# Kernel tuning notes

Measured on AMD Instinct MI355X. Metric: run time of the kernel, lower is better.

Reference implementation:

```python
import jax, jax.numpy as jnp
import numpy as np


def setup_inputs() -> dict:
    key = jax.random.key(0)
    k1, k2 = jax.random.split(key)
    B, H, N, C = 8, 8, 2048, 64
    x = jax.random.normal(k1, (B, H, N, C), dtype=jnp.float32)
    # torch nn.Linear(dim, 3*dim) weight layout: [3C, C]
    W_qkv = jax.random.normal(k2, (3 * C, C), dtype=jnp.float32) * (C ** -0.5)
    return {"x": x, "W_qkv": W_qkv}


def reference(x, W_qkv):
    B, H, N, C = x.shape
    scale = C ** -0.5
    # fused qkv projection: x @ W^T, then split
    qkv = jnp.einsum('bhnc,dc->bhnd', x, W_qkv)  # [B,H,N,3C]
    q, k, v = jnp.split(qkv, 3, axis=-1)
    # full N x N score matrix (matches the naive original)
    attn = jnp.einsum('bhnc,bhmc->bhnm', q, k) * scale
    attn = jax.nn.softmax(attn, axis=-1)
    out = jnp.einsum('bhnm,bhmc->bhnc', attn, v)  # [B,H,N,C]
    # head-mixing shuffle: reshape(B,H,N,H,C//H).transpose(1,3).reshape(B,H,N,C)
    out = out.reshape(B, H, N, H, C // H)
    out = out.transpose(0, 3, 2, 1, 4)
    return out.reshape(B, H, N, C)
```

## Files before the change

### kernel.cpp

```cpp
#include <hip/hip_runtime.h>
#include <math.h>

#define BH    64
#define NSEQ  2048
#define CDIM  64
#define KSTR  72
#define VLS   136

typedef unsigned short ushort_t;
typedef __attribute__((ext_vector_type(8))) short short8;
typedef __attribute__((ext_vector_type(4))) float float4v;

__device__ __forceinline__ ushort_t f32_to_bf16_rne(float x) {
  unsigned int u = __float_as_uint(x);
  u += 0x7fffu + ((u >> 16) & 1u);
  return (ushort_t)(u >> 16);
}

__device__ __forceinline__ void glds16(const ushort_t* g, ushort_t* l) {
  __builtin_amdgcn_global_load_lds(
      (const __attribute__((address_space(1))) void*)g,
      (__attribute__((address_space(3))) void*)l, 16, 0, 0);
}

__global__ __launch_bounds__(256) void qkv_proj_mfma(
    const float* __restrict__ x, const float* __restrict__ w,
    ushort_t* __restrict__ q, ushort_t* __restrict__ k,
    ushort_t* __restrict__ vt) {
  __shared__ ushort_t Wb[192 * KSTR];
  __shared__ ushort_t Vl[64 * VLS];
  const int t = threadIdx.x;
  const int lane = t & 63, wv = t >> 6;
  const int quad = lane >> 4, l16 = lane & 15;
  const long rowbase = (long)blockIdx.x * 128;
  const int head  = (int)(rowbase >> 11);
  const int nbase = (int)(rowbase & 2047);

  for (int u = t; u < 1536; u += 256) {
    const int d = u >> 3, o8 = (u & 7) * 8;
    const float sc = (d < 64) ? 0.1803368801111244f : 1.0f;
    const float4 f0 = *reinterpret_cast<const float4*>(w + d * 64 + o8);
    const float4 f1 = *reinterpret_cast<const float4*>(w + d * 64 + o8 + 4);
    ushort_t tmp[8] __attribute__((aligned(16)));
    tmp[0] = f32_to_bf16_rne(f0.x * sc); tmp[1] = f32_to_bf16_rne(f0.y * sc);
    tmp[2] = f32_to_bf16_rne(f0.z * sc); tmp[3] = f32_to_bf16_rne(f0.w * sc);
    tmp[4] = f32_to_bf16_rne(f1.x * sc); tmp[5] = f32_to_bf16_rne(f1.y * sc);
    tmp[6] = f32_to_bf16_rne(f1.z * sc); tmp[7] = f32_to_bf16_rne(f1.w * sc);
    *reinterpret_cast<uint4*>(&Wb[d * KSTR + o8]) = *reinterpret_cast<const uint4*>(tmp);
  }
  __syncthreads();

  short8 xf[2][2];
#pragma unroll
  for (int tm = 0; tm < 2; ++tm)
#pragma unroll
    for (int kb = 0; kb < 2; ++kb) {
      const float* xp = x + (rowbase + wv * 32 + tm * 16 + l16) * 64 + kb * 32 + quad * 8;
      const float4 f0 = *reinterpret_cast<const float4*>(xp);
      const float4 f1 = *reinterpret_cast<const float4*>(xp + 4);
      ushort_t tmp[8] __attribute__((aligned(16)));
      tmp[0] = f32_to_bf16_rne(f0.x); tmp[1] = f32_to_bf16_rne(f0.y);
      tmp[2] = f32_to_bf16_rne(f0.z); tmp[3] = f32_to_bf16_rne(f0.w);
      tmp[4] = f32_to_bf16_rne(f1.x); tmp[5] = f32_to_bf16_rne(f1.y);
      tmp[6] = f32_to_bf16_rne(f1.z); tmp[7] = f32_to_bf16_rne(f1.w);
      xf[tm][kb] = *reinterpret_cast<const short8*>(tmp);
    }

  float4v acc[2][12];
#pragma unroll
  for (int tm = 0; tm < 2; ++tm)
#pragma unroll
    for (int nt = 0; nt < 12; ++nt)
#pragma unroll
      for (int r = 0; r < 4; ++r) acc[tm][nt][r] = 0.f;

#pragma unroll
  for (int kb = 0; kb < 2; ++kb)
#pragma unroll
    for (int nt = 0; nt < 12; ++nt) {
      const short8 wf = *reinterpret_cast<const short8*>(
          &Wb[(nt * 16 + l16) * KSTR + kb * 32 + quad * 8]);
      acc[0][nt] = __builtin_amdgcn_mfma_f32_16x16x32_bf16(xf[0][kb], wf, acc[0][nt], 0, 0, 0);
      acc[1][nt] = __builtin_amdgcn_mfma_f32_16x16x32_bf16(xf[1][kb], wf, acc[1][nt], 0, 0, 0);
    }

#pragma unroll
  for (int tm = 0; tm < 2; ++tm)
#pragma unroll
    for (int nt = 0; nt < 12; ++nt)
#pragma unroll
      for (int r = 0; r < 4; ++r) {
        const int row_local = wv * 32 + tm * 16 + quad * 4 + r;
        const ushort_t val = f32_to_bf16_rne(acc[tm][nt][r]);
        const int d = nt * 16 + l16;
        if (nt < 4)      q[(rowbase + row_local) * 64 + d] = val;
        else if (nt < 8) k[(rowbase + row_local) * 64 + (d - 64)] = val;
        else             Vl[(d - 128) * VLS + row_local] = val;
      }
  __syncthreads();

#pragma unroll
  for (int i = 0; i < 4; ++i) {
    const int uidx = t + i * 256;
    const int c = uidx >> 4, n0 = (uidx & 15) * 8;
    *reinterpret_cast<uint4*>(vt + (long)head * (64 * 2048) + (long)c * 2048 + nbase + n0) =
        *reinterpret_cast<const uint4*>(&Vl[c * VLS + n0]);
  }
}

__global__ __launch_bounds__(256, 3) void flash_attn_mfma(
    const ushort_t* __restrict__ q, const ushort_t* __restrict__ k,
    const ushort_t* __restrict__ vt, float* __restrict__ out) {
  __shared__ ushort_t Ks2[2][64 * 64];
  __shared__ ushort_t Vs2[2][64 * 64];
  __shared__ ushort_t Ps[128 * KSTR];
  const int t = threadIdx.x;
  const int lane = t & 63, w = t >> 6;
  const int quad = lane >> 4, l16 = lane & 15;
  const int id = blockIdx.x;
  const int qt = id >> 6;
  const int bh = ((id & 7) << 3) | ((id >> 3) & 7);
  const long hoff = (long)bh * NSEQ * CDIM;
  const ushort_t* qp  = q  + hoff + (long)qt * 128 * CDIM;
  const ushort_t* kp  = k  + hoff;
  const ushort_t* vtp = vt + hoff;

  short8 qf[2][2];
#pragma unroll
  for (int tm = 0; tm < 2; ++tm)
#pragma unroll
    for (int kb = 0; kb < 2; ++kb)
      qf[tm][kb] = *reinterpret_cast<const short8*>(
          qp + (w * 32 + tm * 16 + l16) * 64 + kb * 32 + quad * 8);

  float4v O[4][2];
  float rs[2];
#pragma unroll
  for (int tm = 0; tm < 2; ++tm) rs[tm] = 0.f;
#pragma unroll
  for (int ct = 0; ct < 4; ++ct)
#pragma unroll
    for (int tm = 0; tm < 2; ++tm)
#pragma unroll
      for (int r = 0; r < 4; ++r) O[ct][tm][r] = 0.f;

  const int srow = w * 16 + (lane >> 3);
  const int schk = (lane & 7) ^ (lane >> 3);
  const int sdst = w * 16 * 64;

#pragma unroll
  for (int j = 0; j < 2; ++j) {
    glds16(kp + (long)(srow + j * 8) * 64 + schk * 8, &Ks2[0][sdst + j * 512]);
    glds16(vtp + (long)(srow + j * 8) * 2048 + schk * 8, &Vs2[0][sdst + j * 512]);
  }

  for (int tile = 0; tile < NSEQ / 64; ++tile) {
    const int cur = tile & 1;
    __syncthreads();
    if (tile < NSEQ / 64 - 1) {
      const long nxt = tile + 1;
#pragma unroll
      for (int j = 0; j < 2; ++j) {
        glds16(kp + (nxt * 64 + srow + j * 8) * 64 + schk * 8,
               &Ks2[1 - cur][sdst + j * 512]);
        glds16(vtp + (long)(srow + j * 8) * 2048 + nxt * 64 + schk * 8,
               &Vs2[1 - cur][sdst + j * 512]);
      }
    }

    float4v s[4][2];
#pragma unroll
    for (int nt = 0; nt < 4; ++nt)
#pragma unroll
      for (int tm = 0; tm < 2; ++tm)
#pragma unroll
        for (int r = 0; r < 4; ++r) s[nt][tm][r] = 0.f;

#pragma unroll
    for (int kb = 0; kb < 2; ++kb) {
      short8 kf[4];
#pragma unroll
      for (int nt = 0; nt < 4; ++nt)
        kf[nt] = *reinterpret_cast<const short8*>(
            &Ks2[cur][(nt * 16 + l16) * 64 + (((kb * 4 + quad) ^ (l16 & 7)) * 8)]);
#pragma unroll
      for (int nt = 0; nt < 4; ++nt)
#pragma unroll
        for (int tm = 0; tm < 2; ++tm)
          s[nt][tm] = __builtin_amdgcn_mfma_f32_16x16x32_bf16(
              kf[nt], qf[tm][kb], s[nt][tm], 0, 0, 0);
    }

#pragma unroll
    for (int tm = 0; tm < 2; ++tm)
#pragma unroll
      for (int nt = 0; nt < 4; ++nt) {
        float p0 = __builtin_amdgcn_exp2f(s[nt][tm][0]);
        float p1 = __builtin_amdgcn_exp2f(s[nt][tm][1]);
        float p2 = __builtin_amdgcn_exp2f(s[nt][tm][2]);
        float p3 = __builtin_amdgcn_exp2f(s[nt][tm][3]);
        rs[tm] += (p0 + p1) + (p2 + p3);
        uint2 pk;
        pk.x = ((__float_as_uint(p0) + 0x8000u) >> 16) |
               ((__float_as_uint(p1) + 0x8000u) & 0xffff0000u);
        pk.y = ((__float_as_uint(p2) + 0x8000u) >> 16) |
               ((__float_as_uint(p3) + 0x8000u) & 0xffff0000u);
        *reinterpret_cast<uint2*>(
            &Ps[(w * 32 + tm * 16 + l16) * KSTR + nt * 16 + quad * 4]) = pk;
      }

#pragma unroll
    for (int kb = 0; kb < 2; ++kb) {
      short8 pf[2], vf[4];
#pragma unroll
      for (int tm = 0; tm < 2; ++tm)
        pf[tm] = *reinterpret_cast<const short8*>(
            &Ps[(w * 32 + tm * 16 + l16) * KSTR + kb * 32 + quad * 8]);
#pragma unroll
      for (int ct = 0; ct < 4; ++ct)
        vf[ct] = *reinterpret_cast<const short8*>(
            &Vs2[cur][(ct * 16 + l16) * 64 + (((kb * 4 + quad) ^ (l16 & 7)) * 8)]);
#pragma unroll
      for (int ct = 0; ct < 4; ++ct)
#pragma unroll
        for (int tm = 0; tm < 2; ++tm)
          O[ct][tm] = __builtin_amdgcn_mfma_f32_16x16x32_bf16(
              vf[ct], pf[tm], O[ct][tm], 0, 0, 0);
    }
  }

  const int bi = bh >> 3, h = bh & 7;
  float inv[2];
#pragma unroll
  for (int tm = 0; tm < 2; ++tm) {
    float l = rs[tm];
    l += __shfl_xor(l, 16, 64);
    l += __shfl_xor(l, 32, 64);
    inv[tm] = 1.f / l;
  }
#pragma unroll
  for (int ct = 0; ct < 4; ++ct)
#pragma unroll
    for (int tm = 0; tm < 2; ++tm) {
      const int n = qt * 128 + w * 32 + tm * 16 + l16;
      const int h2 = ct * 2 + (quad >> 1);
      const int c2b = (quad & 1) * 4;
      float4 v4;
      v4.x = O[ct][tm][0] * inv[tm]; v4.y = O[ct][tm][1] * inv[tm];
      v4.z = O[ct][tm][2] * inv[tm]; v4.w = O[ct][tm][3] * inv[tm];
      *reinterpret_cast<float4*>(
          &out[(((long)(bi * 8 + h2)) * NSEQ + n) * 64 + h * 8 + c2b]) = v4;
    }
}

extern "C" void kernel_launch(void* const* d_in, const int* in_sizes, int n_in,
                              void* d_out, int out_size, void* d_ws, size_t ws_size,
                              hipStream_t stream) {
  (void)in_sizes; (void)n_in; (void)out_size; (void)ws_size;
  const float* x = (const float*)d_in[0];
  const float* w = (const float*)d_in[1];
  float* out = (float*)d_out;

  ushort_t* qws  = (ushort_t*)d_ws;
  ushort_t* kws  = qws + (size_t)BH * NSEQ * CDIM;
  ushort_t* vtws = kws + (size_t)BH * NSEQ * CDIM;

  qkv_proj_mfma<<<(BH * NSEQ) / 128, 256, 0, stream>>>(x, w, qws, kws, vtws);
  flash_attn_mfma<<<1024, 256, 0, stream>>>(qws, kws, vtws, out);
}
```

Before: 202.0 us.

## Double query tile per block, shrink KV tile, and transpose projection outputs in registers

The attention kernel now gives each wave 64 query rows (256 per block, 512 blocks) and streams K/V in 32-key tiles with a new swizzled P layout. Each loaded K/V tile is therefore reused across more queries, which cuts LDS and global traffic per FLOP, at the cost of more registers and lower occupancy (launch bound lowered to 2). The projection kernel swaps MFMA operand order so Q/K and transposed V are written as packed 4-element vectors straight from registers. This drops the LDS staging buffer and one barrier. The grid shrinks to 512 blocks, which may leave fewer waves to hide latency on the GPU's many CUs.

```diff
diff --git a/kernel.cpp b/kernel.cpp
--- a/kernel.cpp
+++ b/kernel.cpp
@@ -4,8 +4,7 @@
 #define BH    64
 #define NSEQ  2048
 #define CDIM  64
-#define KSTR  72
-#define VLS   136
+#define WSTR  72
 
 typedef unsigned short ushort_t;
 typedef __attribute__((ext_vector_type(8))) short short8;
@@ -17,6 +16,11 @@
   return (ushort_t)(u >> 16);
 }
 
+__device__ __forceinline__ unsigned int pk2(float a, float b) {
+  return ((__float_as_uint(a) + 0x8000u) >> 16) |
+         ((__float_as_uint(b) + 0x8000u) & 0xffff0000u);
+}
+
 __device__ __forceinline__ void glds16(const ushort_t* g, ushort_t* l) {
   __builtin_amdgcn_global_load_lds(
       (const __attribute__((address_space(1))) void*)g,
@@ -27,8 +31,7 @@
     const float* __restrict__ x, const float* __restrict__ w,
     ushort_t* __restrict__ q, ushort_t* __restrict__ k,
     ushort_t* __restrict__ vt) {
-  __shared__ ushort_t Wb[192 * KSTR];
-  __shared__ ushort_t Vl[64 * VLS];
+  __shared__ ushort_t Wb[192 * WSTR];
   const int t = threadIdx.x;
   const int lane = t & 63, wv = t >> 6;
   const int quad = lane >> 4, l16 = lane & 15;
@@ -46,7 +49,7 @@
     tmp[2] = f32_to_bf16_rne(f0.z * sc); tmp[3] = f32_to_bf16_rne(f0.w * sc);
     tmp[4] = f32_to_bf16_rne(f1.x * sc); tmp[5] = f32_to_bf16_rne(f1.y * sc);
     tmp[6] = f32_to_bf16_rne(f1.z * sc); tmp[7] = f32_to_bf16_rne(f1.w * sc);
-    *reinterpret_cast<uint4*>(&Wb[d * KSTR + o8]) = *reinterpret_cast<const uint4*>(tmp);
+    *reinterpret_cast<uint4*>(&Wb[d * WSTR + o8]) = *reinterpret_cast<const uint4*>(tmp);
   }
   __syncthreads();
 
@@ -66,54 +69,72 @@
       xf[tm][kb] = *reinterpret_cast<const short8*>(tmp);
     }
 
-  float4v acc[2][12];
+  float4v aqk[8][2];
+  float4v av[2][4];
+#pragma unroll
+  for (int nt = 0; nt < 8; ++nt)
+#pragma unroll
+    for (int tm = 0; tm < 2; ++tm)
+#pragma unroll
+      for (int r = 0; r < 4; ++r) aqk[nt][tm][r] = 0.f;
 #pragma unroll
   for (int tm = 0; tm < 2; ++tm)
 #pragma unroll
-    for (int nt = 0; nt < 12; ++nt)
-#pragma unroll
-      for (int r = 0; r < 4; ++r) acc[tm][nt][r] = 0.f;
-
-#pragma unroll
-  for (int kb = 0; kb < 2; ++kb)
-#pragma unroll
-    for (int nt = 0; nt < 12; ++nt) {
+    for (int nt = 0; nt < 4; ++nt)
+#pragma unroll
+      for (int r = 0; r < 4; ++r) av[tm][nt][r] = 0.f;
+
+#pragma unroll
+  for (int kb = 0; kb < 2; ++kb) {
+#pragma unroll
+    for (int nt = 0; nt < 8; ++nt) {
       const short8 wf = *reinterpret_cast<const short8*>(
-          &Wb[(nt * 16 + l16) * KSTR + kb * 32 + quad * 8]);
-      acc[0][nt] = __builtin_amdgcn_mfma_f32_16x16x32_bf16(xf[0][kb], wf, acc[0][nt], 0, 0, 0);
-      acc[1][nt] = __builtin_amdgcn_mfma_f32_16x16x32_bf16(xf[1][kb], wf, acc[1][nt], 0, 0, 0);
-    }
-
+          &Wb[(nt * 16 + l16) * WSTR + kb * 32 + quad * 8]);
+      aqk[nt][0] = __builtin_amdgcn_mfma_f32_16x16x32_bf16(wf, xf[0][kb], aqk[nt][0], 0, 0, 0);
+      aqk[nt][1] = __builtin_amdgcn_mfma_f32_16x16x32_bf16(wf, xf[1][kb], aqk[nt][1], 0, 0, 0);
+    }
+#pragma unroll
+    for (int nt = 0; nt < 4; ++nt) {
+      const short8 wfv = *reinterpret_cast<const short8*>(
+          &Wb[((128 + nt * 16) + l16) * WSTR + kb * 32 + quad * 8]);
+      av[0][nt] = __builtin_amdgcn_mfma_f32_16x16x32_bf16(xf[0][kb], wfv, av[0][nt], 0, 0, 0);
+      av[1][nt] = __builtin_amdgcn_mfma_f32_16x16x32_bf16(xf[1][kb], wfv, av[1][nt], 0, 0, 0);
+    }
+  }
+
+#pragma unroll
+  for (int tm = 0; tm < 2; ++tm) {
+    const long row = rowbase + wv * 32 + tm * 16 + l16;
+#pragma unroll
+    for (int nt = 0; nt < 8; ++nt) {
+      uint2 pk;
+      pk.x = pk2(aqk[nt][tm][0], aqk[nt][tm][1]);
+      pk.y = pk2(aqk[nt][tm][2], aqk[nt][tm][3]);
+      if (nt < 4)
+        *reinterpret_cast<uint2*>(q + row * 64 + nt * 16 + quad * 4) = pk;
+      else
+        *reinterpret_cast<uint2*>(k + row * 64 + (nt - 4) * 16 + quad * 4) = pk;
+    }
+  }
 #pragma unroll
   for (int tm = 0; tm < 2; ++tm)
 #pragma unroll
-    for (int nt = 0; nt < 12; ++nt)
-#pragma unroll
-      for (int r = 0; r < 4; ++r) {
-        const int row_local = wv * 32 + tm * 16 + quad * 4 + r;
-        const ushort_t val = f32_to_bf16_rne(acc[tm][nt][r]);
-        const int d = nt * 16 + l16;
-        if (nt < 4)      q[(rowbase + row_local) * 64 + d] = val;
-        else if (nt < 8) k[(rowbase + row_local) * 64 + (d - 64)] = val;
-        else             Vl[(d - 128) * VLS + row_local] = val;
-      }
-  __syncthreads();
-
-#pragma unroll
-  for (int i = 0; i < 4; ++i) {
-    const int uidx = t + i * 256;
-    const int c = uidx >> 4, n0 = (uidx & 15) * 8;
-    *reinterpret_cast<uint4*>(vt + (long)head * (64 * 2048) + (long)c * 2048 + nbase + n0) =
-        *reinterpret_cast<const uint4*>(&Vl[c * VLS + n0]);
-  }
-}
-
-__global__ __launch_bounds__(256, 3) void flash_attn_mfma(
+    for (int nt = 0; nt < 4; ++nt) {
+      const int c = nt * 16 + l16;
+      uint2 pk;
+      pk.x = pk2(av[tm][nt][0], av[tm][nt][1]);
+      pk.y = pk2(av[tm][nt][2], av[tm][nt][3]);
+      *reinterpret_cast<uint2*>(vt + (long)head * (64 * 2048) + (long)c * 2048 +
+                                nbase + wv * 32 + tm * 16 + quad * 4) = pk;
+    }
+}
+
+__global__ __launch_bounds__(256, 2) void flash_attn_mfma(
     const ushort_t* __restrict__ q, const ushort_t* __restrict__ k,
     const ushort_t* __restrict__ vt, float* __restrict__ out) {
-  __shared__ ushort_t Ks2[2][64 * 64];
-  __shared__ ushort_t Vs2[2][64 * 64];
-  __shared__ ushort_t Ps[128 * KSTR];
+  __shared__ ushort_t Ks2[2][32 * 64];
+  __shared__ ushort_t Vs2[2][64 * 32];
+  __shared__ ushort_t Ps[256 * 32];
   const int t = threadIdx.x;
   const int lane = t & 63, w = t >> 6;
   const int quad = lane >> 4, l16 = lane & 15;
@@ -121,118 +142,112 @@
   const int qt = id >> 6;
   const int bh = ((id & 7) << 3) | ((id >> 3) & 7);
   const long hoff = (long)bh * NSEQ * CDIM;
-  const ushort_t* qp  = q  + hoff + (long)qt * 128 * CDIM;
+  const ushort_t* qp  = q  + hoff + (long)qt * 256 * CDIM;
   const ushort_t* kp  = k  + hoff;
   const ushort_t* vtp = vt + hoff;
 
-  short8 qf[2][2];
-#pragma unroll
-  for (int tm = 0; tm < 2; ++tm)
+  short8 qf[4][2];
+#pragma unroll
+  for (int tm = 0; tm < 4; ++tm)
 #pragma unroll
     for (int kb = 0; kb < 2; ++kb)
       qf[tm][kb] = *reinterpret_cast<const short8*>(
-          qp + (w * 32 + tm * 16 + l16) * 64 + kb * 32 + quad * 8);
-
-  float4v O[4][2];
-  float rs[2];
-#pragma unroll
-  for (int tm = 0; tm < 2; ++tm) rs[tm] = 0.f;
+          qp + (w * 64 + tm * 16 + l16) * 64 + kb * 32 + quad * 8);
+
+  float4v O[4][4];
+  float rs[4];
+#pragma unroll
+  for (int tm = 0; tm < 4; ++tm) rs[tm] = 0.f;
 #pragma unroll
   for (int ct = 0; ct < 4; ++ct)
 #pragma unroll
-    for (int tm = 0; tm < 2; ++tm)
+    for (int tm = 0; tm < 4; ++tm)
 #pragma unroll
       for (int r = 0; r < 4; ++r) O[ct][tm][r] = 0.f;
 
-  const int srow = w * 16 + (lane >> 3);
-  const int schk = (lane & 7) ^ (lane >> 3);
-  const int sdst = w * 16 * 64;
-
-#pragma unroll
-  for (int j = 0; j < 2; ++j) {
-    glds16(kp + (long)(srow + j * 8) * 64 + schk * 8, &Ks2[0][sdst + j * 512]);
-    glds16(vtp + (long)(srow + j * 8) * 2048 + schk * 8, &Vs2[0][sdst + j * 512]);
-  }
-
-  for (int tile = 0; tile < NSEQ / 64; ++tile) {
+  const int krow = w * 8 + (lane >> 3);
+  const int kchk = (lane & 7) ^ (lane >> 3);
+  const int kdst = w * 8 * 64;
+  const int vrow = w * 16 + (lane >> 2);
+  const int vchk = (lane & 3) ^ ((lane >> 3) & 3);
+  const int vdst = w * 16 * 32;
+  const int pswz = (l16 >> 1) & 3;
+
+  glds16(kp + (long)krow * 64 + kchk * 8, &Ks2[0][kdst]);
+  glds16(vtp + (long)vrow * 2048 + vchk * 8, &Vs2[0][vdst]);
+
+  for (int tile = 0; tile < NSEQ / 32; ++tile) {
     const int cur = tile & 1;
     __syncthreads();
-    if (tile < NSEQ / 64 - 1) {
+    if (tile < NSEQ / 32 - 1) {
       const long nxt = tile + 1;
-#pragma unroll
-      for (int j = 0; j < 2; ++j) {
-        glds16(kp + (nxt * 64 + srow + j * 8) * 64 + schk * 8,
-               &Ks2[1 - cur][sdst + j * 512]);
-        glds16(vtp + (long)(srow + j * 8) * 2048 + nxt * 64 + schk * 8,
-               &Vs2[1 - cur][sdst + j * 512]);
-      }
-    }
-
-    float4v s[4][2];
-#pragma unroll
-    for (int nt = 0; nt < 4; ++nt)
-#pragma unroll
-      for (int tm = 0; tm < 2; ++tm)
+      glds16(kp + (nxt * 32 + krow) * 64 + kchk * 8, &Ks2[1 - cur][kdst]);
+      glds16(vtp + (long)vrow * 2048 + nxt * 32 + vchk * 8, &Vs2[1 - cur][vdst]);
+    }
+
+    float4v s[2][4];
+#pragma unroll
+    for (int nt = 0; nt < 2; ++nt)
+#pragma unroll
+      for (int tm = 0; tm < 4; ++tm)
 #pragma unroll
         for (int r = 0; r < 4; ++r) s[nt][tm][r] = 0.f;
 
 #pragma unroll
     for (int kb = 0; kb < 2; ++kb) {
-      short8 kf[4];
-#pragma unroll
-      for (int nt = 0; nt < 4; ++nt)
+      short8 kf[2];
+#pragma unroll
+      for (int nt = 0; nt < 2; ++nt)
         kf[nt] = *reinterpret_cast<const short8*>(
             &Ks2[cur][(nt * 16 + l16) * 64 + (((kb * 4 + quad) ^ (l16 & 7)) * 8)]);
 #pragma unroll
-      for (int nt = 0; nt < 4; ++nt)
-#pragma unroll
-        for (int tm = 0; tm < 2; ++tm)
+      for (int nt = 0; nt < 2; ++nt)
+#pragma unroll
+        for (int tm = 0; tm < 4; ++tm)
           s[nt][tm] = __builtin_amdgcn_mfma_f32_16x16x32_bf16(
               kf[nt], qf[tm][kb], s[nt][tm], 0, 0, 0);
     }
 
 #pragma unroll
-    for (int tm = 0; tm < 2; ++tm)
-#pragma unroll
-      for (int nt = 0; nt < 4; ++nt) {
-        float p0 = __builtin_amdgcn_exp2f(s[nt][tm][0]);
-        float p1 = __builtin_amdgcn_exp2f(s[nt][tm][1]);
-        float p2 = __builtin_amdgcn_exp2f(s[nt][tm][2]);
-        float p3 = __builtin_amdgcn_exp2f(s[nt][tm][3]);
+    for (int tm = 0; tm < 4; ++tm)
+#pragma unroll
+      for (int nt = 0; nt < 2; ++nt) {
+        const float p0 = __builtin_amdgcn_exp2f(s[nt][tm][0]);
+        const float p1 = __builtin_amdgcn_exp2f(s[nt][tm][1]);
+        const float p2 = __builtin_amdgcn_exp2f(s[nt][tm][2]);
+        const float p3 = __builtin_amdgcn_exp2f(s[nt][tm][3]);
         rs[tm] += (p0 + p1) + (p2 + p3);
         uint2 pk;
-        pk.x = ((__float_as_uint(p0) + 0x8000u) >> 16) |
-               ((__float_as_uint(p1) + 0x8000u) & 0xffff0000u);
-        pk.y = ((__float_as_uint(p2) + 0x8000u) >> 16) |
-               ((__float_as_uint(p3) + 0x8000u) & 0xffff0000u);
+        pk.x = pk2(p0, p1);
+        pk.y = pk2(p2, p3);
         *reinterpret_cast<uint2*>(
-            &Ps[(w * 32 + tm * 16 + l16) * KSTR + nt * 16 + quad * 4]) = pk;
+            &Ps[(w * 64 + tm * 16 + l16) * 32 +
+                (((nt * 2 + (quad >> 1)) ^ pswz) * 8) + (quad & 1) * 4]) = pk;
       }
 
-#pragma unroll
-    for (int kb = 0; kb < 2; ++kb) {
-      short8 pf[2], vf[4];
-#pragma unroll
-      for (int tm = 0; tm < 2; ++tm)
+    {
+      short8 pf[4], vf[4];
+#pragma unroll
+      for (int tm = 0; tm < 4; ++tm)
         pf[tm] = *reinterpret_cast<const short8*>(
-            &Ps[(w * 32 + tm * 16 + l16) * KSTR + kb * 32 + quad * 8]);
+            &Ps[(w * 64 + tm * 16 + l16) * 32 + ((quad ^ pswz) * 8)]);
 #pragma unroll
       for (int ct = 0; ct < 4; ++ct)
         vf[ct] = *reinterpret_cast<const short8*>(
-            &Vs2[cur][(ct * 16 + l16) * 64 + (((kb * 4 + quad) ^ (l16 & 7)) * 8)]);
+            &Vs2[cur][(ct * 16 + l16) * 32 + ((quad ^ pswz) * 8)]);
 #pragma unroll
       for (int ct = 0; ct < 4; ++ct)
 #pragma unroll
-        for (int tm = 0; tm < 2; ++tm)
+        for (int tm = 0; tm < 4; ++tm)
           O[ct][tm] = __builtin_amdgcn_mfma_f32_16x16x32_bf16(
               vf[ct], pf[tm], O[ct][tm], 0, 0, 0);
     }
   }
 
   const int bi = bh >> 3, h = bh & 7;
-  float inv[2];
-#pragma unroll
-  for (int tm = 0; tm < 2; ++tm) {
+  float inv[4];
+#pragma unroll
+  for (int tm = 0; tm < 4; ++tm) {
     float l = rs[tm];
     l += __shfl_xor(l, 16, 64);
     l += __shfl_xor(l, 32, 64);
@@ -241,8 +256,8 @@
 #pragma unroll
   for (int ct = 0; ct < 4; ++ct)
 #pragma unroll
-    for (int tm = 0; tm < 2; ++tm) {
-      const int n = qt * 128 + w * 32 + tm * 16 + l16;
+    for (int tm = 0; tm < 4; ++tm) {
+      const int n = qt * 256 + w * 64 + tm * 16 + l16;
       const int h2 = ct * 2 + (quad >> 1);
       const int c2b = (quad & 1) * 4;
       float4 v4;
@@ -266,5 +281,5 @@
   ushort_t* vtws = kws + (size_t)BH * NSEQ * CDIM;
 
   qkv_proj_mfma<<<(BH * NSEQ) / 128, 256, 0, stream>>>(x, w, qws, kws, vtws);
-  flash_attn_mfma<<<1024, 256, 0, stream>>>(qws, kws, vtws, out);
-}
+  flash_attn_mfma<<<512, 256, 0, stream>>>(qws, kws, vtws, out);
+}
```

New measurement: 181.7 us. -10.1%, faster.
